# Kernel tuning notes

Measured on AMD Instinct MI355X. Metric: run time of the kernel, lower is better.

## Reference

```python
import jax, jax.numpy as jnp
import numpy as np

B, S, E, H, A, V = 64, 256, 512, 512, 512, 50000
PAD = 0


def setup_inputs() -> dict:
    key = jax.random.key(0)
    ks = jax.random.split(key, 12)
    src = jax.random.randint(ks[0], (B, S), 0, V)
    src_lens = jax.random.randint(ks[1], (B,), 1, S + 1)
    asp_hidden = jax.random.normal(ks[2], (B, A), jnp.float32)
    embedding = jax.random.normal(ks[3], (V, E), jnp.float32) * 0.02
    embedding = embedding.at[PAD].set(0.0)  # nn.Embedding padding_idx row is zero
    s = 1.0 / np.sqrt(H)
    u = lambda k, shp: jax.random.uniform(k, shp, jnp.float32, -s, s)
    return {
        'src': src, 'src_lens': src_lens, 'asp_hidden': asp_hidden,
        'embedding': embedding,
        'Wx_f': u(ks[4], (E, 3 * H)), 'Wh_f': u(ks[5], (H, 3 * H)),
        'Wa_f': u(ks[6], (A, 3 * H)), 'b_f': u(ks[7], (3 * H,)),
        'Wx_b': u(ks[8], (E, 3 * H)), 'Wh_b': u(ks[9], (H, 3 * H)),
        'Wa_b': u(ks[10], (A, 3 * H)), 'b_b': u(ks[11], (3 * H,)),
    }


def _gru_scan(xg_seq, h0, Wh):
    # xg_seq: [S, B, 3H] = x@Wx + asp@Wa + b (precomputed, time-major)
    def step(h, xg):
        hg = h @ Wh  # [B, 3H]
        xr, xz, xn = jnp.split(xg, 3, axis=-1)
        hr, hz, hn = jnp.split(hg, 3, axis=-1)
        r = jax.nn.sigmoid(xr + hr)
        z = jax.nn.sigmoid(xz + hz)
        n = jnp.tanh(xn + r * hn)
        h = (1.0 - z) * h + z * n
        return h, h
    hT, outs = jax.lax.scan(step, h0, xg_seq)
    return hT, outs  # [B,H], [S,B,H]


def reference(src, src_lens, asp_hidden, embedding,
              Wx_f, Wh_f, Wa_f, b_f, Wx_b, Wh_b, Wa_b, b_b):
    x = embedding[src]                              # [B, S, E]
    batch = src.shape[0]
    h0 = jnp.zeros((batch, Wh_f.shape[0]), x.dtype)  # zero-init state

    def run(xseq, Wx, Wh, Wa, b):
        asp_g = asp_hidden @ Wa + b                 # [B, 3H], aspect-conditioned gate bias
        xg = jnp.einsum('bse,eg->sbg', xseq, Wx) + asp_g[None]
        return _gru_scan(xg, h0, Wh)

    hT_f, out_f = run(x, Wx_f, Wh_f, Wa_f, b_f)
    hT_b, out_b = run(x[:, ::-1], Wx_b, Wh_b, Wa_b, b_b)
    out_b = out_b[::-1]                             # realign reversed direction

    memory_bank = jnp.concatenate([out_f, out_b], -1).transpose(1, 0, 2)  # [B,S,2H]
    # final_state order is [fwd, bwd]; wrapper cats final[-1] (bwd) then final[-2] (fwd)
    encoder_last = jnp.concatenate([hT_b, hT_f], -1)  # [B, 2H]
    return memory_bank, encoder_last
```

## Files before the change

kernel.cpp:

```cpp
#include <hip/hip_runtime.h>
#include <hip/hip_bf16.h>

typedef __bf16 bf16x8 __attribute__((ext_vector_type(8)));
typedef float f32x4 __attribute__((ext_vector_type(4)));
typedef unsigned int u32;
typedef unsigned short u16;

#define NB 64
#define NS 256
#define NE 512
#define NH 512
#define NG 1536
#define NM (NS*NB)

__device__ __forceinline__ float fsig(float x) { return 1.0f/(1.0f + __expf(-x)); }
__device__ __forceinline__ float ftanh(float x) {
  float ax = fabsf(x);
  float t = __expf(-2.0f*ax);
  float r = (1.0f - t)/(1.0f + t);
  return copysignf(r, x);
}

__global__ __launch_bounds__(256) void k_gather(const int* __restrict__ src,
                                                const float* __restrict__ emb,
                                                __hip_bfloat16* __restrict__ xsb) {
  int row = blockIdx.x*4 + (threadIdx.x >> 6);
  int lane = threadIdx.x & 63;
  int s = row >> 6, b = row & 63;
  int idx = src[b*NS + s];
  const float* erow = emb + (long)idx*NE + lane*8;
  float4 v0 = *(const float4*)erow;
  float4 v1 = *(const float4*)(erow + 4);
  __hip_bfloat16 tmp[8];
  tmp[0]=__float2bfloat16(v0.x); tmp[1]=__float2bfloat16(v0.y);
  tmp[2]=__float2bfloat16(v0.z); tmp[3]=__float2bfloat16(v0.w);
  tmp[4]=__float2bfloat16(v1.x); tmp[5]=__float2bfloat16(v1.y);
  tmp[6]=__float2bfloat16(v1.z); tmp[7]=__float2bfloat16(v1.w);
  *(uint4*)(xsb + (long)row*NE + lane*8) = *(uint4*)tmp;
}

__global__ __launch_bounds__(256) void k_transpose(const float* i0, const float* i1,
                                                   const float* i2, const float* i3,
                                                   __hip_bfloat16* o0, __hip_bfloat16* o1,
                                                   __hip_bfloat16* o2, __hip_bfloat16* o3) {
  const float* in; __hip_bfloat16* out;
  switch (blockIdx.z) {
    case 0: in=i0; out=o0; break;
    case 1: in=i1; out=o1; break;
    case 2: in=i2; out=o2; break;
    default: in=i3; out=o3; break;
  }
  __shared__ float t[32][33];
  int e0 = blockIdx.x*32, g0 = blockIdx.y*32;
  int r = threadIdx.x >> 5, c = threadIdx.x & 31;
  #pragma unroll
  for (int i=0;i<4;i++) t[r+8*i][c] = in[(long)(e0+r+8*i)*NG + g0+c];
  __syncthreads();
  #pragma unroll
  for (int i=0;i<4;i++) out[(long)(g0+r+8*i)*NE + e0+c] = __float2bfloat16(t[c][r+8*i]);
}

__global__ __launch_bounds__(256) void k_aspg(const float* __restrict__ asp,
     const float* __restrict__ Wa_f, const float* __restrict__ bias_f,
     const float* __restrict__ Wa_b, const float* __restrict__ bias_b,
     float* __restrict__ aspg_f, float* __restrict__ aspg_b) {
  int dir = blockIdx.z;
  const float* Wa  = dir ? Wa_b  : Wa_f;
  const float* bia = dir ? bias_b : bias_f;
  float* outp = dir ? aspg_b : aspg_f;
  int g = blockIdx.x*256 + threadIdx.x;
  int b0 = blockIdx.y*8;
  __shared__ float la[8*512];
  #pragma unroll
  for (int i=0;i<16;i++){ int idx=i*256+threadIdx.x; la[idx] = asp[(long)(b0 + (idx>>9))*512 + (idx&511)]; }
  __syncthreads();
  float bv = bia[g];
  float acc[8];
  #pragma unroll
  for (int bb=0;bb<8;bb++) acc[bb]=bv;
  for (int a=0;a<512;a++){
    float w = Wa[(long)a*NG + g];
    #pragma unroll
    for (int bb=0;bb<8;bb++) acc[bb] += la[bb*512+a]*w;
  }
  #pragma unroll
  for (int bb=0;bb<8;bb++) outp[(long)(b0+bb)*NG + g] = acc[bb];
}

__global__ __launch_bounds__(256,3) void k_xgemm(const __hip_bfloat16* __restrict__ A,
                                                 const __hip_bfloat16* __restrict__ WT,
                                                 __hip_bfloat16* __restrict__ C) {
  __shared__ __hip_bfloat16 sA[128*64];
  __shared__ __hip_bfloat16 sB[64*64];
  const int tid = threadIdx.x;
  const int m0 = blockIdx.y*128, n0 = blockIdx.x*64;
  const int wv = tid>>6, lane = tid&63, l16 = lane&15, lq = lane>>4;
  const int wm = wv>>1, wn = wv&1;
  const int srow = tid>>3, sslot = tid&7;
  f32x4 acc[4][2] = {};
  for (int kt=0; kt<8; ++kt) {
    int k0 = kt*64;
    __syncthreads();
    #pragma unroll
    for (int i=0;i<4;i++){
      int row = i*32 + srow;
      const __hip_bfloat16* src = A + (size_t)(m0+row)*512 + k0 + ((sslot ^ (row&7))*8);
      __builtin_amdgcn_global_load_lds(
        (const __attribute__((address_space(1))) void*)src,
        (__attribute__((address_space(3))) void*)((char*)sA + (i*256 + wv*64)*16), 16, 0, 0);
    }
    #pragma unroll
    for (int i=0;i<2;i++){
      int row = i*32 + srow;
      const __hip_bfloat16* src = WT + (size_t)(n0+row)*512 + k0 + ((sslot ^ (row&7))*8);
      __builtin_amdgcn_global_load_lds(
        (const __attribute__((address_space(1))) void*)src,
        (__attribute__((address_space(3))) void*)((char*)sB + (i*256 + wv*64)*16), 16, 0, 0);
    }
    __syncthreads();
    #pragma unroll
    for (int kk=0; kk<64; kk+=32) {
      bf16x8 af[4]; bf16x8 bfv[2];
      #pragma unroll
      for (int mf=0;mf<4;mf++){
        int row = wm*64 + mf*16 + l16;
        int slot = ((kk>>3) + lq) ^ (row&7);
        af[mf] = *(const bf16x8*)((char*)sA + (row*8 + slot)*16);
      }
      #pragma unroll
      for (int nf=0;nf<2;nf++){
        int row = wn*32 + nf*16 + l16;
        int slot = ((kk>>3) + lq) ^ (row&7);
        bfv[nf] = *(const bf16x8*)((char*)sB + (row*8 + slot)*16);
      }
      #pragma unroll
      for (int mf=0;mf<4;mf++)
        #pragma unroll
        for (int nf=0;nf<2;nf++)
          acc[mf][nf] = __builtin_amdgcn_mfma_f32_16x16x32_bf16(af[mf], bfv[nf], acc[mf][nf], 0,0,0);
    }
  }
  #pragma unroll
  for (int mf=0;mf<4;mf++)
    #pragma unroll
    for (int nf=0;nf<2;nf++)
      #pragma unroll
      for (int r=0;r<4;r++){
        int mrow = m0 + wm*64 + mf*16 + lq*4 + r;
        int col = n0 + wn*32 + nf*16 + l16;
        int gate = col >> 9, cin = col & 511;
        int jwg = cin >> 4, c16 = cin & 15;
        C[((size_t)jwg*NM + mrow)*48 + gate*16 + c16] = __float2bfloat16(acc[mf][nf][r]);
      }
}

__global__ __launch_bounds__(256,1) void k_scan(
   const __hip_bfloat16* __restrict__ xg_f, const __hip_bfloat16* __restrict__ xg_b,
   const __hip_bfloat16* __restrict__ whT_f, const __hip_bfloat16* __restrict__ whT_b,
   const float* __restrict__ aspg_f, const float* __restrict__ aspg_b,
   __hip_bfloat16* __restrict__ hbase, u32* __restrict__ flags,
   float* __restrict__ out)
{
  const int dir = blockIdx.y;
  const int jwg = blockIdx.x;
  const int tid = threadIdx.x;
  const int wm = tid>>6, lane = tid&63, l16 = lane&15, lq = lane>>4;
  const __hip_bfloat16* xgd = (dir ? xg_b : xg_f) + (size_t)jwg*NM*48;
  const __hip_bfloat16* whT = dir ? whT_b : whT_f;
  const float* aspg = dir ? aspg_b : aspg_f;
  __hip_bfloat16* hb = hbase + (size_t)dir*2*NB*NH;
  u32* fl = flags + dir*512;

  __shared__ __hip_bfloat16 wl[3*16*512];

  #pragma unroll
  for (int i=0;i<12;i++){
    int cc = i*256 + tid;
    int c = cc>>6, slot = cc&63;
    int gcol = (c>>4)*512 + jwg*16 + (c&15);
    uint4 v = *(const uint4*)(whT + (long)gcol*512 + slot*8);
    *(uint4*)((char*)wl + (c*64 + (slot ^ (c&7)))*16) = v;
  }

  const int jcol = jwg*16 + l16;
  float aspr[3][4];
  float hreg[4] = {0.f,0.f,0.f,0.f};
  #pragma unroll
  for (int g=0; g<3; ++g)
    #pragma unroll
    for (int r=0;r<4;++r){
      int b = wm*16 + lq*4 + r;
      aspr[g][r] = aspg[(long)b*NG + g*512 + jcol];
    }
  __syncthreads();

  float* out2 = out + (long)NB*NS*1024;

  for (int t=0; t<NS; ++t) {
    int s = dir ? (NS-1-t) : t;
    const __hip_bfloat16* xs = xgd + (size_t)s*NB*48;
    __hip_bfloat16 xr[3][4];
    #pragma unroll
    for (int g=0;g<3;++g)
      #pragma unroll
      for (int r=0;r<4;++r){
        int b = wm*16 + lq*4 + r;
        xr[g][r] = xs[b*48 + g*16 + l16];
      }
    __builtin_amdgcn_sched_barrier(0);
    if (t > 0) {
      u32 tgt = (u32)t;
      for (;;) {
        u32 f = 0xffffffffu;
        if (lane < 32)
          f = __hip_atomic_load(fl + lane*16, __ATOMIC_RELAXED, __HIP_MEMORY_SCOPE_AGENT);
        if (__all((int)(f >= tgt))) break;
      }
      __builtin_amdgcn_fence(__ATOMIC_ACQUIRE, "agent");
    }
    const __hip_bfloat16* hin = hb + (t&1)*NB*NH;
    bf16x8 afr[16];
    #pragma unroll
    for (int kc=0;kc<16;++kc)
      afr[kc] = *(const bf16x8*)(hin + (wm*16 + l16)*NH + kc*32 + lq*8);
    f32x4 accg[3] = {};
    #pragma unroll
    for (int kc=0;kc<16;++kc){
      #pragma unroll
      for (int g=0; g<3; ++g){
        int c = g*16 + l16;
        bf16x8 bfr = *(const bf16x8*)((char*)wl + (c*64 + ((kc*4+lq) ^ (c&7)))*16);
        accg[g] = __builtin_amdgcn_mfma_f32_16x16x32_bf16(afr[kc], bfr, accg[g], 0,0,0);
      }
    }
    __hip_bfloat16* hout = hb + ((t+1)&1)*NB*NH;
    #pragma unroll
    for (int r=0;r<4;++r){
      int b = wm*16 + lq*4 + r;
      float rg = fsig(__bfloat162float(xr[0][r]) + aspr[0][r] + accg[0][r]);
      float zg = fsig(__bfloat162float(xr[1][r]) + aspr[1][r] + accg[1][r]);
      float ng = ftanh(__bfloat162float(xr[2][r]) + aspr[2][r] + rg*accg[2][r]);
      float h = (1.f - zg)*hreg[r] + zg*ng;
      hreg[r] = h;
      __hip_bfloat16 hbf = __float2bfloat16(h);
      u16 bits; __builtin_memcpy(&bits, &hbf, 2);
      __hip_atomic_store((u16*)(hout + (long)b*NH + jcol), bits,
                         __ATOMIC_RELAXED, __HIP_MEMORY_SCOPE_AGENT);
    }
    __syncthreads();
    if (tid == 0)
      __hip_atomic_store(fl + jwg*16, (u32)(t+1), __ATOMIC_RELEASE, __HIP_MEMORY_SCOPE_AGENT);
    #pragma unroll
    for (int r=0;r<4;++r){
      int b = wm*16 + lq*4 + r;
      out[((long)b*NS + s)*1024 + dir*512 + jcol] = hreg[r];
    }
  }
  #pragma unroll
  for (int r=0;r<4;++r){
    int b = wm*16 + lq*4 + r;
    out2[(long)b*1024 + (dir ? 0 : 512) + jcol] = hreg[r];
  }
}

extern "C" void kernel_launch(void* const* d_in, const int* in_sizes, int n_in,
                              void* d_out, int out_size, void* d_ws, size_t ws_size,
                              hipStream_t stream) {
  const int*   src  = (const int*)  d_in[0];
  const float* asp  = (const float*)d_in[2];
  const float* emb  = (const float*)d_in[3];
  const float* Wx_f = (const float*)d_in[4];
  const float* Wh_f = (const float*)d_in[5];
  const float* Wa_f = (const float*)d_in[6];
  const float* b_f  = (const float*)d_in[7];
  const float* Wx_b = (const float*)d_in[8];
  const float* Wh_b = (const float*)d_in[9];
  const float* Wa_b = (const float*)d_in[10];
  const float* b_b  = (const float*)d_in[11];

  char* ws = (char*)d_ws;
  size_t o = 0;
  auto alloc = [&](size_t bytes)->char* { char* p = ws + o; o += (bytes + 255) & ~(size_t)255; return p; };
  __hip_bfloat16* xsb    = (__hip_bfloat16*)alloc((size_t)NM*NE*2);
  __hip_bfloat16* wxT_f  = (__hip_bfloat16*)alloc((size_t)NG*NE*2);
  __hip_bfloat16* wxT_b  = (__hip_bfloat16*)alloc((size_t)NG*NE*2);
  __hip_bfloat16* whT_f  = (__hip_bfloat16*)alloc((size_t)NG*NH*2);
  __hip_bfloat16* whT_b  = (__hip_bfloat16*)alloc((size_t)NG*NH*2);
  float*          aspg_f = (float*)alloc((size_t)NB*NG*4);
  float*          aspg_b = (float*)alloc((size_t)NB*NG*4);
  __hip_bfloat16* xg_f   = (__hip_bfloat16*)alloc((size_t)NM*NG*2);
  __hip_bfloat16* xg_b   = (__hip_bfloat16*)alloc((size_t)NM*NG*2);
  __hip_bfloat16* hbuf   = (__hip_bfloat16*)alloc((size_t)2*2*NB*NH*2);
  u32*            flags  = (u32*)alloc((size_t)2*512*4);

  hipMemsetAsync(hbuf, 0, (size_t)2*2*NB*NH*2 + (size_t)2*512*4, stream);

  k_gather<<<dim3(NM/4), 256, 0, stream>>>(src, emb, xsb);
  k_transpose<<<dim3(16,48,4), 256, 0, stream>>>(Wx_f, Wx_b, Wh_f, Wh_b, wxT_f, wxT_b, whT_f, whT_b);
  k_aspg<<<dim3(6,8,2), 256, 0, stream>>>(asp, Wa_f, b_f, Wa_b, b_b, aspg_f, aspg_b);
  k_xgemm<<<dim3(24,128), 256, 0, stream>>>(xsb, wxT_f, xg_f);
  k_xgemm<<<dim3(24,128), 256, 0, stream>>>(xsb, wxT_b, xg_b);
  k_scan<<<dim3(32,2), 256, 0, stream>>>(xg_f, xg_b, whT_f, whT_b, aspg_f, aspg_b,
                                         hbuf, flags, (float*)d_out);
}
```

Measured before the change: 1.949 ms.

## Replace block barrier handoff with per-wave flags and cache-bypassing stores/loads

Each wave now publishes its own completion flag after waiting for its own write-through h stores, which removes the per-step __syncthreads and single-thread release. Consumer waves poll only the flags of the row group they need, packed densely, instead of one flag per workgroup. h loads and stores use inline asm with sc0 sc1 cache bits in place of acquire fences and atomics, aiming to shorten the cross-workgroup latency on each of the 256 serial steps. Correctness now rests on the cache-coherence behaviour of those bits rather than on formal memory-model ordering, which is a risk.

```diff
diff --git a/kernel.cpp b/kernel.cpp
--- a/kernel.cpp
+++ b/kernel.cpp
@@ -20,6 +20,21 @@
   float r = (1.0f - t)/(1.0f + t);
   return copysignf(r, x);
 }
+
+__device__ __forceinline__ void store_u16_wt(void* p, u32 val, int byteoff) {
+  switch (byteoff) {
+    case 0:    asm volatile("global_store_short %0, %1, off sc0 sc1" :: "v"(p), "v"(val) : "memory"); break;
+    case 1024: asm volatile("global_store_short %0, %1, off offset:1024 sc0 sc1" :: "v"(p), "v"(val) : "memory"); break;
+    case 2048: asm volatile("global_store_short %0, %1, off offset:2048 sc0 sc1" :: "v"(p), "v"(val) : "memory"); break;
+    default:   asm volatile("global_store_short %0, %1, off offset:3072 sc0 sc1" :: "v"(p), "v"(val) : "memory"); break;
+  }
+}
+__device__ __forceinline__ void store_u32_wt(void* p, u32 val) {
+  asm volatile("global_store_dword %0, %1, off sc0 sc1" :: "v"(p), "v"(val) : "memory");
+}
+#define HLOAD(dst, off) \
+  asm volatile("global_load_dwordx4 %0, %1, off offset:" off " sc0 sc1" \
+               : "=v"(dst) : "v"(hl) : "memory")
 
 __global__ __launch_bounds__(256) void k_gather(const int* __restrict__ src,
                                                 const float* __restrict__ emb,
@@ -165,11 +180,12 @@
   const int jwg = blockIdx.x;
   const int tid = threadIdx.x;
   const int wm = tid>>6, lane = tid&63, l16 = lane&15, lq = lane>>4;
+  const int mrow = wm*16 + l16;
   const __hip_bfloat16* xgd = (dir ? xg_b : xg_f) + (size_t)jwg*NM*48;
   const __hip_bfloat16* whT = dir ? whT_b : whT_f;
   const float* aspg = dir ? aspg_b : aspg_f;
   __hip_bfloat16* hb = hbase + (size_t)dir*2*NB*NH;
-  u32* fl = flags + dir*512;
+  u32* fl = flags + dir*256;
 
   __shared__ __hip_bfloat16 wl[3*16*512];
 
@@ -194,6 +210,7 @@
     }
   __syncthreads();
 
+  u32* fp = fl + ((lane < 32 ? lane : 0)*4 + wm);
   float* out2 = out + (long)NB*NS*1024;
 
   for (int t=0; t<NS; ++t) {
@@ -209,34 +226,35 @@
       }
     __builtin_amdgcn_sched_barrier(0);
     if (t > 0) {
-      u32 tgt = (u32)t;
+      const u32 tgt = (u32)t;
       for (;;) {
-        u32 f = 0xffffffffu;
-        if (lane < 32)
-          f = __hip_atomic_load(fl + lane*16, __ATOMIC_RELAXED, __HIP_MEMORY_SCOPE_AGENT);
+        u32 f = __hip_atomic_load(fp, __ATOMIC_RELAXED, __HIP_MEMORY_SCOPE_AGENT);
         if (__all((int)(f >= tgt))) break;
       }
-      __builtin_amdgcn_fence(__ATOMIC_ACQUIRE, "agent");
-    }
-    const __hip_bfloat16* hin = hb + (t&1)*NB*NH;
-    bf16x8 afr[16];
-    #pragma unroll
-    for (int kc=0;kc<16;++kc)
-      afr[kc] = *(const bf16x8*)(hin + (wm*16 + l16)*NH + kc*32 + lq*8);
+    }
+    const char* hl = (const char*)(hb + (t&1)*NB*NH) + mrow*1024 + lq*16;
+    uint4 hv[16];
+    HLOAD(hv[0],  "0");   HLOAD(hv[1],  "64");  HLOAD(hv[2],  "128"); HLOAD(hv[3],  "192");
+    HLOAD(hv[4],  "256"); HLOAD(hv[5],  "320"); HLOAD(hv[6],  "384"); HLOAD(hv[7],  "448");
+    HLOAD(hv[8],  "512"); HLOAD(hv[9],  "576"); HLOAD(hv[10], "640"); HLOAD(hv[11], "704");
+    HLOAD(hv[12], "768"); HLOAD(hv[13], "832"); HLOAD(hv[14], "896"); HLOAD(hv[15], "960");
+    asm volatile("s_waitcnt vmcnt(0)" ::: "memory");
+    __builtin_amdgcn_sched_barrier(0);
     f32x4 accg[3] = {};
     #pragma unroll
     for (int kc=0;kc<16;++kc){
+      bf16x8 af;
+      __builtin_memcpy(&af, &hv[kc], 16);
       #pragma unroll
       for (int g=0; g<3; ++g){
         int c = g*16 + l16;
         bf16x8 bfr = *(const bf16x8*)((char*)wl + (c*64 + ((kc*4+lq) ^ (c&7)))*16);
-        accg[g] = __builtin_amdgcn_mfma_f32_16x16x32_bf16(afr[kc], bfr, accg[g], 0,0,0);
-      }
-    }
-    __hip_bfloat16* hout = hb + ((t+1)&1)*NB*NH;
+        accg[g] = __builtin_amdgcn_mfma_f32_16x16x32_bf16(af, bfr, accg[g], 0,0,0);
+      }
+    }
+    char* hs = (char*)(hb + ((t+1)&1)*NB*NH) + (size_t)(wm*16 + lq*4)*1024 + jcol*2;
     #pragma unroll
     for (int r=0;r<4;++r){
-      int b = wm*16 + lq*4 + r;
       float rg = fsig(__bfloat162float(xr[0][r]) + aspr[0][r] + accg[0][r]);
       float zg = fsig(__bfloat162float(xr[1][r]) + aspr[1][r] + accg[1][r]);
       float ng = ftanh(__bfloat162float(xr[2][r]) + aspr[2][r] + rg*accg[2][r]);
@@ -244,12 +262,11 @@
       hreg[r] = h;
       __hip_bfloat16 hbf = __float2bfloat16(h);
       u16 bits; __builtin_memcpy(&bits, &hbf, 2);
-      __hip_atomic_store((u16*)(hout + (long)b*NH + jcol), bits,
-                         __ATOMIC_RELAXED, __HIP_MEMORY_SCOPE_AGENT);
-    }
-    __syncthreads();
-    if (tid == 0)
-      __hip_atomic_store(fl + jwg*16, (u32)(t+1), __ATOMIC_RELEASE, __HIP_MEMORY_SCOPE_AGENT);
+      store_u16_wt(hs, (u32)bits, r*1024);
+    }
+    asm volatile("s_waitcnt vmcnt(0)" ::: "memory");
+    if (lane == 0)
+      store_u32_wt(fl + jwg*4 + wm, (u32)(t+1));
     #pragma unroll
     for (int r=0;r<4;++r){
       int b = wm*16 + lq*4 + r;
@@ -291,9 +308,9 @@
   __hip_bfloat16* xg_f   = (__hip_bfloat16*)alloc((size_t)NM*NG*2);
   __hip_bfloat16* xg_b   = (__hip_bfloat16*)alloc((size_t)NM*NG*2);
   __hip_bfloat16* hbuf   = (__hip_bfloat16*)alloc((size_t)2*2*NB*NH*2);
-  u32*            flags  = (u32*)alloc((size_t)2*512*4);
-
-  hipMemsetAsync(hbuf, 0, (size_t)2*2*NB*NH*2 + (size_t)2*512*4, stream);
+  u32*            flags  = (u32*)alloc((size_t)2*256*4);
+
+  hipMemsetAsync(hbuf, 0, (size_t)2*2*NB*NH*2 + (size_t)2*256*4, stream);
 
   k_gather<<<dim3(NM/4), 256, 0, stream>>>(src, emb, xsb);
   k_transpose<<<dim3(16,48,4), 256, 0, stream>>>(Wx_f, Wx_b, Wh_f, Wh_b, wxT_f, wxT_b, whT_f, whT_b);
```

Result: faster. 1.711 ms (-12.2%).

## Replace persistent flag-synced GRU scan with per-timestep kernel launches

Applied to the files above, without the earlier changes.

The persistent scan kernel, which used global atomic flags to sync workgroups between timesteps, is replaced by 256 separate per-step kernel launches. Kernel boundaries now provide the grid-wide barrier. The hidden state moves to an fp32 buffer and is converted to bf16 on load. The aspect bias is folded into the xgemm epilogue. Each launch reloads the Wh slice into LDS and pays launch overhead, which likely outweighs the cost of the spin-wait it removes.

```diff
diff --git a/kernel.cpp b/kernel.cpp
--- a/kernel.cpp
+++ b/kernel.cpp
@@ -89,6 +89,7 @@
 
 __global__ __launch_bounds__(256,3) void k_xgemm(const __hip_bfloat16* __restrict__ A,
                                                  const __hip_bfloat16* __restrict__ WT,
+                                                 const float* __restrict__ aspg,
                                                  __hip_bfloat16* __restrict__ C) {
   __shared__ __hip_bfloat16 sA[128*64];
   __shared__ __hip_bfloat16 sB[64*64];
@@ -148,28 +149,30 @@
       for (int r=0;r<4;r++){
         int mrow = m0 + wm*64 + mf*16 + lq*4 + r;
         int col = n0 + wn*32 + nf*16 + l16;
+        float v = acc[mf][nf][r] + aspg[(size_t)(mrow & 63)*NG + col];
         int gate = col >> 9, cin = col & 511;
         int jwg = cin >> 4, c16 = cin & 15;
-        C[((size_t)jwg*NM + mrow)*48 + gate*16 + c16] = __float2bfloat16(acc[mf][nf][r]);
-      }
-}
-
-__global__ __launch_bounds__(256,1) void k_scan(
+        C[((size_t)jwg*NM + mrow)*48 + gate*16 + c16] = __float2bfloat16(v);
+      }
+}
+
+__global__ __launch_bounds__(256,1) void k_step(
    const __hip_bfloat16* __restrict__ xg_f, const __hip_bfloat16* __restrict__ xg_b,
    const __hip_bfloat16* __restrict__ whT_f, const __hip_bfloat16* __restrict__ whT_b,
-   const float* __restrict__ aspg_f, const float* __restrict__ aspg_b,
-   __hip_bfloat16* __restrict__ hbase, u32* __restrict__ flags,
-   float* __restrict__ out)
+   float* __restrict__ hbase,
+   float* __restrict__ out, int t)
 {
   const int dir = blockIdx.y;
   const int jwg = blockIdx.x;
   const int tid = threadIdx.x;
   const int wm = tid>>6, lane = tid&63, l16 = lane&15, lq = lane>>4;
+  const int mrow = wm*16 + l16;
+  const int s = dir ? (NS-1-t) : t;
   const __hip_bfloat16* xgd = (dir ? xg_b : xg_f) + (size_t)jwg*NM*48;
   const __hip_bfloat16* whT = dir ? whT_b : whT_f;
-  const float* aspg = dir ? aspg_b : aspg_f;
-  __hip_bfloat16* hb = hbase + (size_t)dir*2*NB*NH;
-  u32* fl = flags + dir*512;
+  float* hb = hbase + (size_t)dir*2*NB*NH;
+  const float* hin = hb + (size_t)(t&1)*NB*NH;
+  float* hout = hb + (size_t)((t+1)&1)*NB*NH;
 
   __shared__ __hip_bfloat16 wl[3*16*512];
 
@@ -183,83 +186,59 @@
   }
 
   const int jcol = jwg*16 + l16;
-  float aspr[3][4];
-  float hreg[4] = {0.f,0.f,0.f,0.f};
-  #pragma unroll
-  for (int g=0; g<3; ++g)
+  const __hip_bfloat16* xs = xgd + (size_t)s*NB*48;
+  __hip_bfloat16 xr[3][4];
+  #pragma unroll
+  for (int g=0;g<3;++g)
     #pragma unroll
     for (int r=0;r<4;++r){
       int b = wm*16 + lq*4 + r;
-      aspr[g][r] = aspg[(long)b*NG + g*512 + jcol];
-    }
-  __syncthreads();
-
-  float* out2 = out + (long)NB*NS*1024;
-
-  for (int t=0; t<NS; ++t) {
-    int s = dir ? (NS-1-t) : t;
-    const __hip_bfloat16* xs = xgd + (size_t)s*NB*48;
-    __hip_bfloat16 xr[3][4];
-    #pragma unroll
-    for (int g=0;g<3;++g)
-      #pragma unroll
-      for (int r=0;r<4;++r){
-        int b = wm*16 + lq*4 + r;
-        xr[g][r] = xs[b*48 + g*16 + l16];
-      }
-    __builtin_amdgcn_sched_barrier(0);
-    if (t > 0) {
-      u32 tgt = (u32)t;
-      for (;;) {
-        u32 f = 0xffffffffu;
-        if (lane < 32)
-          f = __hip_atomic_load(fl + lane*16, __ATOMIC_RELAXED, __HIP_MEMORY_SCOPE_AGENT);
-        if (__all((int)(f >= tgt))) break;
-      }
-      __builtin_amdgcn_fence(__ATOMIC_ACQUIRE, "agent");
-    }
-    const __hip_bfloat16* hin = hb + (t&1)*NB*NH;
-    bf16x8 afr[16];
-    #pragma unroll
-    for (int kc=0;kc<16;++kc)
-      afr[kc] = *(const bf16x8*)(hin + (wm*16 + l16)*NH + kc*32 + lq*8);
-    f32x4 accg[3] = {};
+      xr[g][r] = xs[b*48 + g*16 + l16];
+    }
+
+  f32x4 accg[3] = {};
+  float hprev[4] = {0.f,0.f,0.f,0.f};
+  if (t > 0) {
+    #pragma unroll
+    for (int r=0;r<4;++r)
+      hprev[r] = hin[(size_t)(wm*16 + lq*4 + r)*NH + jcol];
+    const float* hrow = hin + (size_t)mrow*NH;
+    __syncthreads();
     #pragma unroll
     for (int kc=0;kc<16;++kc){
+      float4 a = *(const float4*)(hrow + kc*32 + lq*8);
+      float4 b2 = *(const float4*)(hrow + kc*32 + lq*8 + 4);
+      u16 tmp[8];
+      __hip_bfloat16 cv;
+      cv = __float2bfloat16(a.x);  __builtin_memcpy(&tmp[0], &cv, 2);
+      cv = __float2bfloat16(a.y);  __builtin_memcpy(&tmp[1], &cv, 2);
+      cv = __float2bfloat16(a.z);  __builtin_memcpy(&tmp[2], &cv, 2);
+      cv = __float2bfloat16(a.w);  __builtin_memcpy(&tmp[3], &cv, 2);
+      cv = __float2bfloat16(b2.x); __builtin_memcpy(&tmp[4], &cv, 2);
+      cv = __float2bfloat16(b2.y); __builtin_memcpy(&tmp[5], &cv, 2);
+      cv = __float2bfloat16(b2.z); __builtin_memcpy(&tmp[6], &cv, 2);
+      cv = __float2bfloat16(b2.w); __builtin_memcpy(&tmp[7], &cv, 2);
+      bf16x8 af; __builtin_memcpy(&af, tmp, 16);
       #pragma unroll
       for (int g=0; g<3; ++g){
         int c = g*16 + l16;
         bf16x8 bfr = *(const bf16x8*)((char*)wl + (c*64 + ((kc*4+lq) ^ (c&7)))*16);
-        accg[g] = __builtin_amdgcn_mfma_f32_16x16x32_bf16(afr[kc], bfr, accg[g], 0,0,0);
-      }
-    }
-    __hip_bfloat16* hout = hb + ((t+1)&1)*NB*NH;
-    #pragma unroll
-    for (int r=0;r<4;++r){
-      int b = wm*16 + lq*4 + r;
-      float rg = fsig(__bfloat162float(xr[0][r]) + aspr[0][r] + accg[0][r]);
-      float zg = fsig(__bfloat162float(xr[1][r]) + aspr[1][r] + accg[1][r]);
-      float ng = ftanh(__bfloat162float(xr[2][r]) + aspr[2][r] + rg*accg[2][r]);
-      float h = (1.f - zg)*hreg[r] + zg*ng;
-      hreg[r] = h;
-      __hip_bfloat16 hbf = __float2bfloat16(h);
-      u16 bits; __builtin_memcpy(&bits, &hbf, 2);
-      __hip_atomic_store((u16*)(hout + (long)b*NH + jcol), bits,
-                         __ATOMIC_RELAXED, __HIP_MEMORY_SCOPE_AGENT);
-    }
-    __syncthreads();
-    if (tid == 0)
-      __hip_atomic_store(fl + jwg*16, (u32)(t+1), __ATOMIC_RELEASE, __HIP_MEMORY_SCOPE_AGENT);
-    #pragma unroll
-    for (int r=0;r<4;++r){
-      int b = wm*16 + lq*4 + r;
-      out[((long)b*NS + s)*1024 + dir*512 + jcol] = hreg[r];
-    }
-  }
+        accg[g] = __builtin_amdgcn_mfma_f32_16x16x32_bf16(af, bfr, accg[g], 0,0,0);
+      }
+    }
+  }
+  float* out2 = out + (size_t)NB*NS*1024;
   #pragma unroll
   for (int r=0;r<4;++r){
     int b = wm*16 + lq*4 + r;
-    out2[(long)b*1024 + (dir ? 0 : 512) + jcol] = hreg[r];
+    float rg = fsig(__bfloat162float(xr[0][r]) + accg[0][r]);
+    float zg = fsig(__bfloat162float(xr[1][r]) + accg[1][r]);
+    float ng = ftanh(__bfloat162float(xr[2][r]) + rg*accg[2][r]);
+    float h = (1.f - zg)*hprev[r] + zg*ng;
+    hout[(size_t)b*NH + jcol] = h;
+    out[((size_t)b*NS + s)*1024 + dir*512 + jcol] = h;
+    if (t == NS-1)
+      out2[(size_t)b*1024 + (dir ? 0 : 512) + jcol] = h;
   }
 }
 
@@ -290,16 +269,14 @@
   float*          aspg_b = (float*)alloc((size_t)NB*NG*4);
   __hip_bfloat16* xg_f   = (__hip_bfloat16*)alloc((size_t)NM*NG*2);
   __hip_bfloat16* xg_b   = (__hip_bfloat16*)alloc((size_t)NM*NG*2);
-  __hip_bfloat16* hbuf   = (__hip_bfloat16*)alloc((size_t)2*2*NB*NH*2);
-  u32*            flags  = (u32*)alloc((size_t)2*512*4);
-
-  hipMemsetAsync(hbuf, 0, (size_t)2*2*NB*NH*2 + (size_t)2*512*4, stream);
+  float*          hbuf32 = (float*)alloc((size_t)2*2*NB*NH*4);
 
   k_gather<<<dim3(NM/4), 256, 0, stream>>>(src, emb, xsb);
   k_transpose<<<dim3(16,48,4), 256, 0, stream>>>(Wx_f, Wx_b, Wh_f, Wh_b, wxT_f, wxT_b, whT_f, whT_b);
   k_aspg<<<dim3(6,8,2), 256, 0, stream>>>(asp, Wa_f, b_f, Wa_b, b_b, aspg_f, aspg_b);
-  k_xgemm<<<dim3(24,128), 256, 0, stream>>>(xsb, wxT_f, xg_f);
-  k_xgemm<<<dim3(24,128), 256, 0, stream>>>(xsb, wxT_b, xg_b);
-  k_scan<<<dim3(32,2), 256, 0, stream>>>(xg_f, xg_b, whT_f, whT_b, aspg_f, aspg_b,
-                                         hbuf, flags, (float*)d_out);
-}
+  k_xgemm<<<dim3(24,128), 256, 0, stream>>>(xsb, wxT_f, aspg_f, xg_f);
+  k_xgemm<<<dim3(24,128), 256, 0, stream>>>(xsb, wxT_b, aspg_b, xg_b);
+  for (int t = 0; t < NS; ++t)
+    k_step<<<dim3(32,2), 256, 0, stream>>>(xg_f, xg_b, whT_f, whT_b,
+                                           hbuf32, (float*)d_out, t);
+}
```

Result: slower. 2.234 ms (+14.6%).
